# Optimization experiments

Hardware: AMD Instinct MI355X
Metric: run time of the kernel (lower is better)

The kernel has to match this reference:

```python
import jax, jax.numpy as jnp
import numpy as np

N_NODES = 50000
D = 128            # input_dim == hidden_dim == output_dim
N_EDGES = 800000   # 2 relation types concatenated
BN_EPS = 1e-5


def _gcn_conv(x, W, b, src, dst, n):
    # PyG GCNConv: add self loops, symmetric normalization, gather-scatter aggregate.
    h = x @ W                                   # [N, D]
    loop = jnp.arange(n)
    s = jnp.concatenate([src, loop])
    d = jnp.concatenate([dst, loop])
    deg = jax.ops.segment_sum(jnp.ones_like(s, dtype=h.dtype), d, num_segments=n)
    dinv = jnp.where(deg > 0, jax.lax.rsqrt(deg), 0.0)
    norm = dinv[s] * dinv[d]                    # [E+N]
    agg = jax.ops.segment_sum(h[s] * norm[:, None], d, num_segments=n)  # [N, D]
    return agg + b


def _batch_norm(x, gamma, beta):
    # BatchNorm1d training-mode math (biased variance over node axis)
    m = x.mean(axis=0)
    v = x.var(axis=0)
    return (x - m) * jax.lax.rsqrt(v + BN_EPS) * gamma + beta


def _gcn_layer(x, src, dst, W, b, gamma, beta, n):
    h = _gcn_conv(x, W, b, src, dst, n)
    h = jax.nn.relu(_batch_norm(h, gamma, beta))
    return h + x  # residual (in_features == out_features); dropout = identity (eval)


def setup_inputs() -> dict:
    key = jax.random.key(0)
    ks = jax.random.split(key, 8)
    x = jax.random.normal(ks[0], (N_NODES, D), dtype=jnp.float32)
    edge_index = jax.random.randint(ks[1], (2, N_EDGES), 0, N_NODES, dtype=jnp.int64)
    sc = 1.0 / np.sqrt(D)
    return {
        "x": x,
        "edge_index": edge_index,
        "W1": jax.random.normal(ks[2], (D, D), dtype=jnp.float32) * sc,
        "b1": jnp.zeros((D,), dtype=jnp.float32),
        "g1": jnp.ones((D,), dtype=jnp.float32),
        "be1": jnp.zeros((D,), dtype=jnp.float32),
        "W2": jax.random.normal(ks[3], (D, D), dtype=jnp.float32) * sc,
        "b2": jnp.zeros((D,), dtype=jnp.float32),
        "g2": jnp.ones((D,), dtype=jnp.float32),
        "be2": jnp.zeros((D,), dtype=jnp.float32),
        "Wa": jax.random.normal(ks[4], (D, 1), dtype=jnp.float32) * sc,
        "ba": jnp.zeros((1,), dtype=jnp.float32),
    }


def reference(x, edge_index, W1, b1, g1, be1, W2, b2, g2, be2, Wa, ba):
    n = x.shape[0]
    src, dst = edge_index[0], edge_index[1]
    h = _gcn_layer(x, src, dst, W1, b1, g1, be1, n)
    h = _gcn_layer(h, src, dst, W2, b2, g2, be2, n)
    att = jax.nn.softmax(jnp.tanh(h @ Wa + ba), axis=0)  # softmax over nodes
    return h * att
```

## Files before the change

kernel.cpp:

```cpp
#include <hip/hip_runtime.h>
#include <hip/hip_fp16.h>

#define NN 50000
#define DD 128
#define NE 800000
#define BN_EPS 1e-5f
#define NBUCK 196
#define TILE_A 4096

typedef _Float16 f16x8 __attribute__((ext_vector_type(8)));
typedef float f32x4 __attribute__((ext_vector_type(4)));

__global__ void k_hist(const int* __restrict__ dst, int* __restrict__ cnt, int ne) {
    int i = blockIdx.x * blockDim.x + threadIdx.x;
    if (i < ne) atomicAdd(&cnt[dst[i]], 1);
}

__global__ __launch_bounds__(256) void k_bsum(const int* __restrict__ cnt,
                                              int* __restrict__ bsum, int n) {
    __shared__ int red[256];
    int i = blockIdx.x * 256 + threadIdx.x;
    int v = (i < n) ? cnt[i] : 0;
    red[threadIdx.x] = v;
    __syncthreads();
    for (int off = 128; off > 0; off >>= 1) {
        if (threadIdx.x < off) red[threadIdx.x] += red[threadIdx.x + off];
        __syncthreads();
    }
    if (threadIdx.x == 0) bsum[blockIdx.x] = red[0];
}

__global__ __launch_bounds__(256) void k_bscan(int* __restrict__ bsum, int nb) {
    __shared__ int sh[256];
    int t = threadIdx.x;
    sh[t] = (t < nb) ? bsum[t] : 0;
    __syncthreads();
    for (int off = 1; off < 256; off <<= 1) {
        int add = (t >= off) ? sh[t - off] : 0;
        __syncthreads();
        sh[t] += add;
        __syncthreads();
    }
    if (t < nb) bsum[t] = sh[t];
}

__global__ __launch_bounds__(256) void k_rowp(const int* __restrict__ cnt,
                                              const int* __restrict__ bsum,
                                              int* __restrict__ rowp,
                                              int* __restrict__ cursor,
                                              int* __restrict__ bucketCur,
                                              float* __restrict__ dinv,
                                              float* __restrict__ sumsZ, int n) {
    if (blockIdx.x == 0) {
        for (int i = threadIdx.x; i < 8256; i += 256) sumsZ[i] = 0.f;
    }
    __shared__ int sh[256];
    int t = threadIdx.x;
    int i = blockIdx.x * 256 + t;
    int v = (i < n) ? cnt[i] : 0;
    sh[t] = v;
    __syncthreads();
    for (int off = 1; off < 256; off <<= 1) {
        int add = (t >= off) ? sh[t - off] : 0;
        __syncthreads();
        sh[t] += add;
        __syncthreads();
    }
    int base = (blockIdx.x > 0) ? bsum[blockIdx.x - 1] : 0;
    int excl = base + sh[t] - v;
    if (i < n) {
        rowp[i] = excl;
        cursor[i] = excl;
        dinv[i] = 1.0f / sqrtf((float)(v + 1));
        if ((i & 255) == 0) bucketCur[i >> 8] = excl;
        if (i == n - 1) rowp[n] = excl + v;
    }
}

__global__ __launch_bounds__(256) void k_binA(const int* __restrict__ src,
                                              const int* __restrict__ dst,
                                              const float* __restrict__ dinv,
                                              int* __restrict__ bucketCur,
                                              uint2* __restrict__ evS, int ne) {
    __shared__ int hcnt[NBUCK];
    __shared__ int hbase[NBUCK];
    int tid = threadIdx.x;
    for (int i = tid; i < NBUCK; i += 256) hcnt[i] = 0;
    __syncthreads();
    int base = blockIdx.x * TILE_A;
    int lim = ne - base;
    if (lim > TILE_A) lim = TILE_A;
    for (int i = tid; i < lim; i += 256) {
        int d = dst[base + i];
        atomicAdd(&hcnt[d >> 8], 1);
    }
    __syncthreads();
    for (int b = tid; b < NBUCK; b += 256) {
        hbase[b] = atomicAdd(&bucketCur[b], hcnt[b]);
        hcnt[b] = 0;
    }
    __syncthreads();
    for (int i = tid; i < lim; i += 256) {
        int d = dst[base + i];
        int s = src[base + i];
        int bk = d >> 8;
        int rank = atomicAdd(&hcnt[bk], 1);
        int pos = hbase[bk] + rank;
        unsigned short hv = __half_as_ushort(__float2half_rn(dinv[s]));
        evS[pos] = make_uint2((unsigned)s | ((unsigned)(d & 255) << 16),
                              (unsigned)hv);
    }
}

__global__ __launch_bounds__(256) void k_binB(const uint2* __restrict__ evS,
                                              const int* __restrict__ rowp,
                                              int* __restrict__ cursor,
                                              unsigned* __restrict__ ev, int n) {
    int b = blockIdx.x;
    int node0 = b << 8;
    int lo = rowp[node0];
    int nhi = node0 + 256;
    if (nhi > n) nhi = n;
    int hi = rowp[nhi];
    for (int p = lo + (int)threadIdx.x; p < hi; p += 256) {
        uint2 r = evS[p];
        int node = node0 + (int)(r.x >> 16);
        int pos = atomicAdd(&cursor[node], 1);
        ev[pos] = (r.x & 0xFFFFu) | (r.y << 16);
    }
}

__global__ __launch_bounds__(256) void k_wprep(const float* __restrict__ W1,
                                               const float* __restrict__ W2,
                                               __half* __restrict__ Wf) {
    int widx = blockIdx.x & 1;
    const float* W = widx ? W2 : W1;
    __half* outp = Wf + (size_t)widx * DD * DD;
    int s = (blockIdx.x >> 1) * 256 + threadIdx.x;
    int l = s & 63;
    int ks = (s >> 6) & 3;
    int cb = s >> 8;
    int col = cb * 16 + (l & 15);
    int kbase = ks * 32 + (l >> 4) * 8;
    __align__(16) __half tmp[8];
    #pragma unroll
    for (int j = 0; j < 8; j++) tmp[j] = __float2half_rn(W[(kbase + j) * DD + col]);
    *(uint4*)(outp + s * 8) = *(uint4*)tmp;
}

#define GTILE 64
__global__ __launch_bounds__(256) void k_gemm(const float* __restrict__ A,
                                              const __half* __restrict__ Wf,
                                              __half* __restrict__ C, int n) {
    __shared__ __half sW[DD * DD];
    __shared__ __half sA[GTILE * DD];
    int tid = threadIdx.x;
    int wave = tid >> 6;
    int lane = tid & 63;

    {
        const float4* wg = (const float4*)Wf;
        float4* ws = (float4*)sW;
        for (int i = tid; i < DD * DD / 8; i += 256) ws[i] = wg[i];
    }

    int ntiles = (n + GTILE - 1) / GTILE;
    for (int t = blockIdx.x; t < ntiles; t += gridDim.x) {
        int row0 = t * GTILE;
        __syncthreads();
        {
            const float4* Av = (const float4*)(A + (size_t)row0 * DD);
            for (int i = tid; i < GTILE * DD / 4; i += 256) {
                int r = i >> 5;
                int kq = i & 31;
                float4 v = make_float4(0.f, 0.f, 0.f, 0.f);
                if (row0 + r < n) v = Av[i];
                __half2 p0 = __floats2half2_rn(v.x, v.y);
                __half2 p1 = __floats2half2_rn(v.z, v.w);
                uint2 pk;
                pk.x = *(unsigned*)&p0;
                pk.y = *(unsigned*)&p1;
                int slot = ((r >> 4) * 4 + (kq >> 3)) * 64 +
                           (((kq >> 1) & 3) << 4) + (r & 15);
                int byte = slot * 16 + (kq & 1) * 8;
                byte ^= ((byte >> 9) & 7) << 4;
                *(uint2*)((char*)sA + byte) = pk;
            }
        }
        __syncthreads();

        f32x4 acc[8];
        #pragma unroll
        for (int cb = 0; cb < 8; cb++) acc[cb] = (f32x4)(0.0f);
        f16x8 af[4];
        #pragma unroll
        for (int ks = 0; ks < 4; ks++) {
            int rb = ((wave * 4 + ks) * 64 + lane) * 16;
            rb ^= ((rb >> 9) & 7) << 4;
            af[ks] = *(const f16x8*)((const char*)sA + rb);
        }
        #pragma unroll
        for (int cb = 0; cb < 8; cb++) {
            #pragma unroll
            for (int ks = 0; ks < 4; ks++) {
                f16x8 bf = *(const f16x8*)(sW + ((cb * 4 + ks) * 64 + lane) * 8);
                acc[cb] = __builtin_amdgcn_mfma_f32_16x16x32_f16(af[ks], bf,
                                                                 acc[cb], 0, 0, 0);
            }
        }

        __half* sC = sA + wave * (16 * DD);
        #pragma unroll
        for (int cb = 0; cb < 8; cb++) {
            int col = cb * 16 + (lane & 15);
            #pragma unroll
            for (int rr = 0; rr < 4; rr++) {
                int grow = (lane >> 4) * 4 + rr;
                sC[grow * DD + (col ^ ((grow & 3) << 4))] = __float2half(acc[cb][rr]);
            }
        }
        __syncthreads();
        #pragma unroll
        for (int i2 = 0; i2 < 4; i2++) {
            int o = (i2 * 64 + lane) * 8;
            int grow = o >> 7;
            int col0 = o & 127;
            int row = row0 + wave * 16 + grow;
            if (row < n) {
                uint4 val = *(uint4*)(sC + grow * DD + (col0 ^ ((grow & 3) << 4)));
                *(uint4*)(C + (size_t)row * DD + col0) = val;
            }
        }
    }
}

__global__ __launch_bounds__(256) void k_agg(const __half* __restrict__ h,
                                             const int* __restrict__ rowp,
                                             const unsigned* __restrict__ ev,
                                             const float* __restrict__ dinv,
                                             const float* __restrict__ bias,
                                             float* __restrict__ out,
                                             float* __restrict__ sums, int n) {
    int tid = threadIdx.x;
    int grp = tid >> 4;
    int m = tid & 15;
    int node = blockIdx.x * 16 + grp;
    bool activ = node < n;

    int beg = 0, end = 0;
    float di = 0.f;
    if (activ) { beg = rowp[node]; end = rowp[node + 1]; di = dinv[node]; }

    float sf[8] = {0.f, 0.f, 0.f, 0.f, 0.f, 0.f, 0.f, 0.f};
    float bf[8];
    {
        float4 b0 = *(const float4*)(bias + m * 8);
        float4 b1 = *(const float4*)(bias + m * 8 + 4);
        bf[0] = b0.x; bf[1] = b0.y; bf[2] = b0.z; bf[3] = b0.w;
        bf[4] = b1.x; bf[5] = b1.y; bf[6] = b1.z; bf[7] = b1.w;
        if (activ) {
            float4 raw = *(const float4*)(h + (size_t)node * DD + m * 8);
            const __half2* hp = (const __half2*)&raw;
            float2 s0 = __half22float2(hp[0]);
            float2 s1 = __half22float2(hp[1]);
            float2 s2 = __half22float2(hp[2]);
            float2 s3 = __half22float2(hp[3]);
            sf[0] = s0.x; sf[1] = s0.y; sf[2] = s1.x; sf[3] = s1.y;
            sf[4] = s2.x; sf[5] = s2.y; sf[6] = s3.x; sf[7] = s3.y;
        }
    }

    float a[8] = {0.f, 0.f, 0.f, 0.f, 0.f, 0.f, 0.f, 0.f};
    #pragma unroll 4
    for (int e = beg; e < end; e++) {
        unsigned r = ev[e];
        int s = r & 0xFFFF;
        float ww = __half2float(__ushort_as_half((unsigned short)(r >> 16)));
        float4 raw = *(const float4*)(h + (size_t)s * DD + m * 8);
        const __half2* hp = (const __half2*)&raw;
        float2 c0 = __half22float2(hp[0]);
        float2 c1 = __half22float2(hp[1]);
        float2 c2 = __half22float2(hp[2]);
        float2 c3 = __half22float2(hp[3]);
        a[0] += ww * c0.x; a[1] += ww * c0.y;
        a[2] += ww * c1.x; a[3] += ww * c1.y;
        a[4] += ww * c2.x; a[5] += ww * c2.y;
        a[6] += ww * c3.x; a[7] += ww * c3.y;
    }

    float o[8];
    float dii = di * di;
    #pragma unroll
    for (int j = 0; j < 8; j++) o[j] = di * a[j] + dii * sf[j] + bf[j];
    if (activ) {
        float* op = out + (size_t)node * DD + m * 8;
        *(float4*)op = make_float4(o[0], o[1], o[2], o[3]);
        *(float4*)(op + 4) = make_float4(o[4], o[5], o[6], o[7]);
    }

    __shared__ float rs[16][132];
    #pragma unroll
    for (int j = 0; j < 8; j++) rs[grp][m * 8 + j] = activ ? o[j] : 0.f;
    __syncthreads();

    int bank = blockIdx.x & 15;
    if (tid < 128) {
        float s = 0.f;
        #pragma unroll
        for (int r2 = 0; r2 < 16; r2++) s += rs[r2][tid];
        atomicAdd(&sums[bank * 256 + tid], s);
    } else {
        int f = tid - 128;
        float q = 0.f;
        #pragma unroll
        for (int r2 = 0; r2 < 16; r2++) { float v = rs[r2][f]; q += v * v; }
        atomicAdd(&sums[bank * 256 + 128 + f], q);
    }
}

__global__ __launch_bounds__(256) void k_bn(const float* __restrict__ X,
                                            const float* __restrict__ res,
                                            const float* __restrict__ sums,
                                            const float* __restrict__ gamma,
                                            const float* __restrict__ beta,
                                            const float* __restrict__ Wa,
                                            const float* __restrict__ ba,
                                            float* __restrict__ out,
                                            float* __restrict__ evec,
                                            float* __restrict__ Zb, int n) {
    __shared__ float s_scale[128], s_shift[128];
    if (threadIdx.x < 128) {
        int ff = threadIdx.x;
        float ssum = 0.f, qsum = 0.f;
        #pragma unroll
        for (int b = 0; b < 16; b++) {
            ssum += sums[b * 256 + ff];
            qsum += sums[b * 256 + 128 + ff];
        }
        float inv_n = 1.0f / (float)n;
        float mean = ssum * inv_n;
        float var = qsum * inv_n - mean * mean;
        float sc = gamma[ff] * (1.0f / sqrtf(var + BN_EPS));
        s_scale[ff] = sc;
        s_shift[ff] = beta[ff] - mean * sc;
    }
    __syncthreads();
    int idx = blockIdx.x * 256 + threadIdx.x;
    int total = n * (DD / 4);
    int f = (threadIdx.x & 31) * 4;
    float o[4] = {0.f, 0.f, 0.f, 0.f};
    if (idx < total) {
        float4 v = ((const float4*)X)[idx];
        float4 rv = ((const float4*)res)[idx];
        float vi[4] = {v.x, v.y, v.z, v.w};
        float ri[4] = {rv.x, rv.y, rv.z, rv.w};
        #pragma unroll
        for (int j = 0; j < 4; j++) {
            float x = vi[j] * s_scale[f + j] + s_shift[f + j];
            x = fmaxf(x, 0.f);
            o[j] = x + ri[j];
        }
        ((float4*)out)[idx] = make_float4(o[0], o[1], o[2], o[3]);
    }
    if (Wa != nullptr) {
        float t = 0.f;
        if (idx < total) {
            float4 wv = *(const float4*)(Wa + f);
            t = o[0] * wv.x + o[1] * wv.y + o[2] * wv.z + o[3] * wv.w;
        }
        #pragma unroll
        for (int m = 16; m >= 1; m >>= 1) t += __shfl_xor(t, m);
        __shared__ float part[8];
        if ((threadIdx.x & 31) == 0) {
            float ev = 0.f;
            if (idx < total) {
                ev = expf(tanhf(t + ba[0]));
                evec[idx >> 5] = ev;
            }
            part[threadIdx.x >> 5] = ev;
        }
        __syncthreads();
        if (threadIdx.x == 0) {
            float z = part[0] + part[1] + part[2] + part[3] +
                      part[4] + part[5] + part[6] + part[7];
            atomicAdd(&Zb[blockIdx.x & 63], z);
        }
    }
}

__global__ __launch_bounds__(256) void k_out(const float* __restrict__ H,
                                             const float* __restrict__ evec,
                                             const float* __restrict__ Zb,
                                             float* __restrict__ out, int n) {
    __shared__ float sZ;
    if (threadIdx.x == 0) {
        float z = 0.f;
        #pragma unroll
        for (int i = 0; i < 64; i++) z += Zb[i];
        sZ = z;
    }
    __syncthreads();
    int idx = blockIdx.x * blockDim.x + threadIdx.x;
    int total = n * (DD / 4);
    if (idx >= total) return;
    int node = idx >> 5;
    float s = evec[node] / sZ;
    float4 h = ((const float4*)H)[idx];
    ((float4*)out)[idx] = make_float4(h.x * s, h.y * s, h.z * s, h.w * s);
}

extern "C" void kernel_launch(void* const* d_in, const int* in_sizes, int n_in,
                              void* d_out, int out_size, void* d_ws, size_t ws_size,
                              hipStream_t stream) {
    const float* x   = (const float*)d_in[0];
    const int* eidx  = (const int*)d_in[1];
    const float* W1  = (const float*)d_in[2];
    const float* b1  = (const float*)d_in[3];
    const float* g1  = (const float*)d_in[4];
    const float* be1 = (const float*)d_in[5];
    const float* W2  = (const float*)d_in[6];
    const float* b2  = (const float*)d_in[7];
    const float* g2  = (const float*)d_in[8];
    const float* be2 = (const float*)d_in[9];
    const float* Wa  = (const float*)d_in[10];
    const float* ba  = (const float*)d_in[11];
    float* out = (float*)d_out;

    const int* srcp = eidx;
    const int* dstp = eidx + NE;

    float* bufA = (float*)d_ws;
    float* bufB = bufA + (size_t)NN * DD;
    float* bufC = bufB + (size_t)NN * DD;
    unsigned* ev = (unsigned*)(bufC + (size_t)NN * DD);
    float* dinv = (float*)(ev + NE);
    float* evec = dinv + NN;
    float* sums = evec + NN;
    float* Zb   = sums + 8192;
    int* cnt    = (int*)(Zb + 64);
    int* rowp   = cnt + NN;
    int* cursor = rowp + NN + 64;
    int* bsum   = cursor + NN;
    int* bucketCur = bsum + 256;
    __half* Wf  = (__half*)(bucketCur + 256);

    __half* hH  = (__half*)bufA;
    uint2* evS  = (uint2*)bufB;

    float* sumsL1 = sums;
    float* sumsL2 = sums + 4096;

    const int nscan = (NN + 255) / 256;

    k_wprep<<<16, 256, 0, stream>>>(W1, W2, Wf);

    hipMemsetAsync(cnt, 0, (size_t)NN * sizeof(int), stream);
    k_hist<<<(NE + 255) / 256, 256, 0, stream>>>(dstp, cnt, NE);
    k_bsum<<<nscan, 256, 0, stream>>>(cnt, bsum, NN);
    k_bscan<<<1, 256, 0, stream>>>(bsum, nscan);
    k_rowp<<<nscan, 256, 0, stream>>>(cnt, bsum, rowp, cursor, bucketCur, dinv,
                                      sums, NN);
    k_binA<<<(NE + TILE_A - 1) / TILE_A, 256, 0, stream>>>(srcp, dstp, dinv,
                                                           bucketCur, evS, NE);
    k_binB<<<NBUCK, 256, 0, stream>>>(evS, rowp, cursor, ev, NN);

    int gemm_grid = (NN + GTILE - 1) / GTILE;
    int agg_grid  = (NN + 15) / 16;
    int ew_grid   = (NN * (DD / 4) + 255) / 256;

    k_gemm<<<gemm_grid, 256, 0, stream>>>(x, Wf, hH, NN);
    k_agg<<<agg_grid, 256, 0, stream>>>(hH, rowp, ev, dinv, b1, bufB, sumsL1, NN);
    k_bn<<<ew_grid, 256, 0, stream>>>(bufB, x, sumsL1, g1, be1, nullptr, nullptr,
                                      bufC, nullptr, nullptr, NN);

    k_gemm<<<gemm_grid, 256, 0, stream>>>(bufC, Wf + (size_t)DD * DD, hH, NN);
    k_agg<<<agg_grid, 256, 0, stream>>>(hH, rowp, ev, dinv, b2, bufB, sumsL2, NN);
    k_bn<<<ew_grid, 256, 0, stream>>>(bufB, bufC, sumsL2, g2, be2, Wa, ba,
                                      bufC, evec, Zb, NN);

    k_out<<<ew_grid, 256, 0, stream>>>(bufC, evec, Zb, out, NN);
}
```

Measured before the change: 318.4 us.

## Fuse layer-1 BatchNorm/ReLU/residual into GEMM prologue and degree-sort aggregation nodes

```diff
diff --git a/kernel.cpp b/kernel.cpp
--- a/kernel.cpp
+++ b/kernel.cpp
@@ -50,12 +50,15 @@
                                               int* __restrict__ cursor,
                                               int* __restrict__ bucketCur,
                                               float* __restrict__ dinv,
-                                              float* __restrict__ sumsZ, int n) {
+                                              float* __restrict__ sumsZ,
+                                              int* __restrict__ dcnt, int n) {
     if (blockIdx.x == 0) {
         for (int i = threadIdx.x; i < 8256; i += 256) sumsZ[i] = 0.f;
     }
     __shared__ int sh[256];
+    __shared__ int dh[64];
     int t = threadIdx.x;
+    if (t < 64) dh[t] = 0;
     int i = blockIdx.x * 256 + t;
     int v = (i < n) ? cnt[i] : 0;
     sh[t] = v;
@@ -74,6 +77,50 @@
         dinv[i] = 1.0f / sqrtf((float)(v + 1));
         if ((i & 255) == 0) bucketCur[i >> 8] = excl;
         if (i == n - 1) rowp[n] = excl + v;
+        atomicAdd(&dh[v > 63 ? 63 : v], 1);
+    }
+    __syncthreads();
+    if (t < 64 && dh[t]) atomicAdd(&dcnt[t], dh[t]);
+}
+
+__global__ __launch_bounds__(64) void k_dscan(const int* __restrict__ dcnt,
+                                              int* __restrict__ dcur) {
+    __shared__ int sh[64];
+    int t = threadIdx.x;
+    sh[t] = dcnt[t];
+    __syncthreads();
+    for (int off = 1; off < 64; off <<= 1) {
+        int add = (t >= off) ? sh[t - off] : 0;
+        __syncthreads();
+        sh[t] += add;
+        __syncthreads();
+    }
+    dcur[t] = sh[t] - dcnt[t];
+}
+
+__global__ __launch_bounds__(256) void k_dperm(const int* __restrict__ cnt,
+                                               int* __restrict__ dcur,
+                                               int* __restrict__ perm, int n) {
+    __shared__ int dh[64], db[64];
+    int t = threadIdx.x;
+    if (t < 64) dh[t] = 0;
+    __syncthreads();
+    int i = blockIdx.x * 256 + t;
+    int b = 0;
+    if (i < n) {
+        int v = cnt[i];
+        b = v > 63 ? 63 : v;
+        atomicAdd(&dh[b], 1);
+    }
+    __syncthreads();
+    if (t < 64) {
+        db[t] = dh[t] ? atomicAdd(&dcur[t], dh[t]) : 0;
+        dh[t] = 0;
+    }
+    __syncthreads();
+    if (i < n) {
+        int r = atomicAdd(&dh[b], 1);
+        perm[db[b] + r] = i;
     }
 }
 
@@ -150,19 +197,40 @@
 
 #define GTILE 64
 __global__ __launch_bounds__(256) void k_gemm(const float* __restrict__ A,
+                                              const float* __restrict__ res,
+                                              const float* __restrict__ sums,
+                                              const float* __restrict__ gamma,
+                                              const float* __restrict__ beta,
+                                              float* __restrict__ Hout,
                                               const __half* __restrict__ Wf,
                                               __half* __restrict__ C, int n) {
     __shared__ __half sW[DD * DD];
     __shared__ __half sA[GTILE * DD];
+    __shared__ float s_scale[DD], s_shift[DD];
     int tid = threadIdx.x;
     int wave = tid >> 6;
     int lane = tid & 63;
+    bool fused = (res != nullptr);
 
     {
         const float4* wg = (const float4*)Wf;
         float4* ws = (float4*)sW;
         for (int i = tid; i < DD * DD / 8; i += 256) ws[i] = wg[i];
     }
+    if (fused && tid < DD) {
+        float ssum = 0.f, qsum = 0.f;
+        #pragma unroll
+        for (int b = 0; b < 16; b++) {
+            ssum += sums[b * 256 + tid];
+            qsum += sums[b * 256 + 128 + tid];
+        }
+        float inv_n = 1.0f / (float)n;
+        float mean = ssum * inv_n;
+        float var = qsum * inv_n - mean * mean;
+        float sc = gamma[tid] * (1.0f / sqrtf(var + BN_EPS));
+        s_scale[tid] = sc;
+        s_shift[tid] = beta[tid] - mean * sc;
+    }
 
     int ntiles = (n + GTILE - 1) / GTILE;
     for (int t = blockIdx.x; t < ntiles; t += gridDim.x) {
@@ -170,11 +238,24 @@
         __syncthreads();
         {
             const float4* Av = (const float4*)(A + (size_t)row0 * DD);
+            const float4* Rv = (const float4*)(res + (size_t)row0 * DD);
+            float4* Hv = (float4*)(Hout + (size_t)row0 * DD);
             for (int i = tid; i < GTILE * DD / 4; i += 256) {
                 int r = i >> 5;
                 int kq = i & 31;
+                bool rowok = (row0 + r < n);
                 float4 v = make_float4(0.f, 0.f, 0.f, 0.f);
-                if (row0 + r < n) v = Av[i];
+                if (rowok) v = Av[i];
+                if (fused) {
+                    float4 rv = make_float4(0.f, 0.f, 0.f, 0.f);
+                    if (rowok) rv = Rv[i];
+                    int f4 = kq * 4;
+                    v.x = fmaxf(v.x * s_scale[f4]     + s_shift[f4],     0.f) + rv.x;
+                    v.y = fmaxf(v.y * s_scale[f4 + 1] + s_shift[f4 + 1], 0.f) + rv.y;
+                    v.z = fmaxf(v.z * s_scale[f4 + 2] + s_shift[f4 + 2], 0.f) + rv.z;
+                    v.w = fmaxf(v.w * s_scale[f4 + 3] + s_shift[f4 + 3], 0.f) + rv.w;
+                    if (rowok) Hv[i] = v;
+                }
                 __half2 p0 = __floats2half2_rn(v.x, v.y);
                 __half2 p1 = __floats2half2_rn(v.z, v.w);
                 uint2 pk;
@@ -238,14 +319,16 @@
                                              const int* __restrict__ rowp,
                                              const unsigned* __restrict__ ev,
                                              const float* __restrict__ dinv,
+                                             const int* __restrict__ perm,
                                              const float* __restrict__ bias,
                                              float* __restrict__ out,
                                              float* __restrict__ sums, int n) {
     int tid = threadIdx.x;
     int grp = tid >> 4;
     int m = tid & 15;
-    int node = blockIdx.x * 16 + grp;
-    bool activ = node < n;
+    int idx = blockIdx.x * 16 + grp;
+    bool activ = idx < n;
+    int node = activ ? perm[idx] : 0;
 
     int beg = 0, end = 0;
     float di = 0.f;
@@ -438,11 +521,14 @@
     float* sums = evec + NN;
     float* Zb   = sums + 8192;
     int* cnt    = (int*)(Zb + 64);
-    int* rowp   = cnt + NN;
+    int* dcnt   = cnt + NN;
+    int* dcur   = dcnt + 64;
+    int* rowp   = dcur + 64;
     int* cursor = rowp + NN + 64;
     int* bsum   = cursor + NN;
     int* bucketCur = bsum + 256;
-    __half* Wf  = (__half*)(bucketCur + 256);
+    int* perm   = bucketCur + 256;
+    __half* Wf  = (__half*)(perm + NN);
 
     __half* hH  = (__half*)bufA;
     uint2* evS  = (uint2*)bufB;
@@ -454,27 +540,31 @@
 
     k_wprep<<<16, 256, 0, stream>>>(W1, W2, Wf);
 
-    hipMemsetAsync(cnt, 0, (size_t)NN * sizeof(int), stream);
+    hipMemsetAsync(cnt, 0, (size_t)(NN + 64) * sizeof(int), stream);
     k_hist<<<(NE + 255) / 256, 256, 0, stream>>>(dstp, cnt, NE);
     k_bsum<<<nscan, 256, 0, stream>>>(cnt, bsum, NN);
     k_bscan<<<1, 256, 0, stream>>>(bsum, nscan);
     k_rowp<<<nscan, 256, 0, stream>>>(cnt, bsum, rowp, cursor, bucketCur, dinv,
-                                      sums, NN);
+                                      sums, dcnt, NN);
     k_binA<<<(NE + TILE_A - 1) / TILE_A, 256, 0, stream>>>(srcp, dstp, dinv,
                                                            bucketCur, evS, NE);
     k_binB<<<NBUCK, 256, 0, stream>>>(evS, rowp, cursor, ev, NN);
+    k_dscan<<<1, 64, 0, stream>>>(dcnt, dcur);
+    k_dperm<<<nscan, 256, 0, stream>>>(cnt, dcur, perm, NN);
 
     int gemm_grid = (NN + GTILE - 1) / GTILE;
     int agg_grid  = (NN + 15) / 16;
     int ew_grid   = (NN * (DD / 4) + 255) / 256;
 
-    k_gemm<<<gemm_grid, 256, 0, stream>>>(x, Wf, hH, NN);
-    k_agg<<<agg_grid, 256, 0, stream>>>(hH, rowp, ev, dinv, b1, bufB, sumsL1, NN);
-    k_bn<<<ew_grid, 256, 0, stream>>>(bufB, x, sumsL1, g1, be1, nullptr, nullptr,
-                                      bufC, nullptr, nullptr, NN);
-
-    k_gemm<<<gemm_grid, 256, 0, stream>>>(bufC, Wf + (size_t)DD * DD, hH, NN);
-    k_agg<<<agg_grid, 256, 0, stream>>>(hH, rowp, ev, dinv, b2, bufB, sumsL2, NN);
+    k_gemm<<<gemm_grid, 256, 0, stream>>>(x, nullptr, nullptr, nullptr, nullptr,
+                                          nullptr, Wf, hH, NN);
+    k_agg<<<agg_grid, 256, 0, stream>>>(hH, rowp, ev, dinv, perm, b1, bufB,
+                                        sumsL1, NN);
+
+    k_gemm<<<gemm_grid, 256, 0, stream>>>(bufB, x, sumsL1, g1, be1, bufC,
+                                          Wf + (size_t)DD * DD, hH, NN);
+    k_agg<<<agg_grid, 256, 0, stream>>>(hH, rowp, ev, dinv, perm, b2, bufB,
+                                        sumsL2, NN);
     k_bn<<<ew_grid, 256, 0, stream>>>(bufB, bufC, sumsL2, g2, be2, Wa, ba,
                                       bufC, evec, Zb, NN);
 
```

New measurement: 320.1 us. Within noise of the previous version (+0.5%).

## Fuse layer-1 BatchNorm into layer-2 GEMM and prescale rows by dinv

Applied to the files above, without the earlier changes.

```diff
diff --git a/kernel.cpp b/kernel.cpp
--- a/kernel.cpp
+++ b/kernel.cpp
@@ -79,9 +79,8 @@
 
 __global__ __launch_bounds__(256) void k_binA(const int* __restrict__ src,
                                               const int* __restrict__ dst,
-                                              const float* __restrict__ dinv,
                                               int* __restrict__ bucketCur,
-                                              uint2* __restrict__ evS, int ne) {
+                                              unsigned* __restrict__ evS, int ne) {
     __shared__ int hcnt[NBUCK];
     __shared__ int hbase[NBUCK];
     int tid = threadIdx.x;
@@ -105,14 +104,11 @@
         int s = src[base + i];
         int bk = d >> 8;
         int rank = atomicAdd(&hcnt[bk], 1);
-        int pos = hbase[bk] + rank;
-        unsigned short hv = __half_as_ushort(__float2half_rn(dinv[s]));
-        evS[pos] = make_uint2((unsigned)s | ((unsigned)(d & 255) << 16),
-                              (unsigned)hv);
-    }
-}
-
-__global__ __launch_bounds__(256) void k_binB(const uint2* __restrict__ evS,
+        evS[hbase[bk] + rank] = (unsigned)s | ((unsigned)(d & 255) << 16);
+    }
+}
+
+__global__ __launch_bounds__(256) void k_binB(const unsigned* __restrict__ evS,
                                               const int* __restrict__ rowp,
                                               int* __restrict__ cursor,
                                               unsigned* __restrict__ ev, int n) {
@@ -123,10 +119,10 @@
     if (nhi > n) nhi = n;
     int hi = rowp[nhi];
     for (int p = lo + (int)threadIdx.x; p < hi; p += 256) {
-        uint2 r = evS[p];
-        int node = node0 + (int)(r.x >> 16);
+        unsigned r = evS[p];
+        int node = node0 + (int)(r >> 16);
         int pos = atomicAdd(&cursor[node], 1);
-        ev[pos] = (r.x & 0xFFFFu) | (r.y << 16);
+        ev[pos] = r & 0xFFFFu;
     }
 }
 
@@ -150,19 +146,41 @@
 
 #define GTILE 64
 __global__ __launch_bounds__(256) void k_gemm(const float* __restrict__ A,
+                                              const float* __restrict__ res,
+                                              const float* __restrict__ sums,
+                                              const float* __restrict__ gamma,
+                                              const float* __restrict__ beta,
+                                              float* __restrict__ Hout,
+                                              const float* __restrict__ dscale,
                                               const __half* __restrict__ Wf,
                                               __half* __restrict__ C, int n) {
     __shared__ __half sW[DD * DD];
     __shared__ __half sA[GTILE * DD];
+    __shared__ float s_scale[DD], s_shift[DD];
     int tid = threadIdx.x;
     int wave = tid >> 6;
     int lane = tid & 63;
+    bool fused = (res != nullptr);
 
     {
         const float4* wg = (const float4*)Wf;
         float4* ws = (float4*)sW;
         for (int i = tid; i < DD * DD / 8; i += 256) ws[i] = wg[i];
     }
+    if (fused && tid < DD) {
+        float ssum = 0.f, qsum = 0.f;
+        #pragma unroll
+        for (int b = 0; b < 16; b++) {
+            ssum += sums[b * 256 + tid];
+            qsum += sums[b * 256 + 128 + tid];
+        }
+        float inv_n = 1.0f / (float)n;
+        float mean = ssum * inv_n;
+        float var = qsum * inv_n - mean * mean;
+        float sc = gamma[tid] * (1.0f / sqrtf(var + BN_EPS));
+        s_scale[tid] = sc;
+        s_shift[tid] = beta[tid] - mean * sc;
+    }
 
     int ntiles = (n + GTILE - 1) / GTILE;
     for (int t = blockIdx.x; t < ntiles; t += gridDim.x) {
@@ -170,11 +188,24 @@
         __syncthreads();
         {
             const float4* Av = (const float4*)(A + (size_t)row0 * DD);
+            const float4* Rv = (const float4*)(res + (size_t)row0 * DD);
+            float4* Hv = (float4*)(Hout + (size_t)row0 * DD);
             for (int i = tid; i < GTILE * DD / 4; i += 256) {
                 int r = i >> 5;
                 int kq = i & 31;
+                bool rowok = (row0 + r < n);
                 float4 v = make_float4(0.f, 0.f, 0.f, 0.f);
-                if (row0 + r < n) v = Av[i];
+                if (rowok) v = Av[i];
+                if (fused) {
+                    float4 rv = make_float4(0.f, 0.f, 0.f, 0.f);
+                    if (rowok) rv = Rv[i];
+                    int f4 = kq * 4;
+                    v.x = fmaxf(v.x * s_scale[f4]     + s_shift[f4],     0.f) + rv.x;
+                    v.y = fmaxf(v.y * s_scale[f4 + 1] + s_shift[f4 + 1], 0.f) + rv.y;
+                    v.z = fmaxf(v.z * s_scale[f4 + 2] + s_shift[f4 + 2], 0.f) + rv.z;
+                    v.w = fmaxf(v.w * s_scale[f4 + 3] + s_shift[f4 + 3], 0.f) + rv.w;
+                    if (rowok) Hv[i] = v;
+                }
                 __half2 p0 = __floats2half2_rn(v.x, v.y);
                 __half2 p1 = __floats2half2_rn(v.z, v.w);
                 uint2 pk;
@@ -209,6 +240,13 @@
             }
         }
 
+        float dv[4];
+        #pragma unroll
+        for (int rr = 0; rr < 4; rr++) {
+            int row = row0 + wave * 16 + (lane >> 4) * 4 + rr;
+            dv[rr] = (row < n) ? dscale[row] : 1.f;
+        }
+
         __half* sC = sA + wave * (16 * DD);
         #pragma unroll
         for (int cb = 0; cb < 8; cb++) {
@@ -216,7 +254,8 @@
             #pragma unroll
             for (int rr = 0; rr < 4; rr++) {
                 int grow = (lane >> 4) * 4 + rr;
-                sC[grow * DD + (col ^ ((grow & 3) << 4))] = __float2half(acc[cb][rr]);
+                sC[grow * DD + (col ^ ((grow & 3) << 4))] =
+                    __float2half(acc[cb][rr] * dv[rr]);
             }
         }
         __syncthreads();
@@ -233,6 +272,12 @@
         }
     }
 }
+
+#define ACC8(raw) { const __half2* hp_ = (const __half2*)&(raw);               \
+    float2 c0_ = __half22float2(hp_[0]); float2 c1_ = __half22float2(hp_[1]);  \
+    float2 c2_ = __half22float2(hp_[2]); float2 c3_ = __half22float2(hp_[3]);  \
+    a[0] += c0_.x; a[1] += c0_.y; a[2] += c1_.x; a[3] += c1_.y;                \
+    a[4] += c2_.x; a[5] += c2_.y; a[6] += c3_.x; a[7] += c3_.y; }
 
 __global__ __launch_bounds__(256) void k_agg(const __half* __restrict__ h,
                                              const int* __restrict__ rowp,
@@ -271,27 +316,36 @@
     }
 
     float a[8] = {0.f, 0.f, 0.f, 0.f, 0.f, 0.f, 0.f, 0.f};
-    #pragma unroll 4
-    for (int e = beg; e < end; e++) {
-        unsigned r = ev[e];
-        int s = r & 0xFFFF;
-        float ww = __half2float(__ushort_as_half((unsigned short)(r >> 16)));
+    int e = beg;
+    int cnt4 = (end - beg) >> 2;
+    if (cnt4 > 0) {
+        unsigned s0 = ev[e], s1 = ev[e + 1], s2 = ev[e + 2], s3 = ev[e + 3];
+        float4 r0 = *(const float4*)(h + (size_t)s0 * DD + m * 8);
+        float4 r1 = *(const float4*)(h + (size_t)s1 * DD + m * 8);
+        float4 r2 = *(const float4*)(h + (size_t)s2 * DD + m * 8);
+        float4 r3 = *(const float4*)(h + (size_t)s3 * DD + m * 8);
+        for (int g = 1; g < cnt4; g++) {
+            e += 4;
+            unsigned t0 = ev[e], t1 = ev[e + 1], t2 = ev[e + 2], t3 = ev[e + 3];
+            float4 q0 = *(const float4*)(h + (size_t)t0 * DD + m * 8);
+            float4 q1 = *(const float4*)(h + (size_t)t1 * DD + m * 8);
+            float4 q2 = *(const float4*)(h + (size_t)t2 * DD + m * 8);
+            float4 q3 = *(const float4*)(h + (size_t)t3 * DD + m * 8);
+            ACC8(r0); ACC8(r1); ACC8(r2); ACC8(r3);
+            r0 = q0; r1 = q1; r2 = q2; r3 = q3;
+        }
+        ACC8(r0); ACC8(r1); ACC8(r2); ACC8(r3);
+        e += 4;
+    }
+    for (; e < end; e++) {
+        unsigned s = ev[e];
         float4 raw = *(const float4*)(h + (size_t)s * DD + m * 8);
-        const __half2* hp = (const __half2*)&raw;
-        float2 c0 = __half22float2(hp[0]);
-        float2 c1 = __half22float2(hp[1]);
-        float2 c2 = __half22float2(hp[2]);
-        float2 c3 = __half22float2(hp[3]);
-        a[0] += ww * c0.x; a[1] += ww * c0.y;
-        a[2] += ww * c1.x; a[3] += ww * c1.y;
-        a[4] += ww * c2.x; a[5] += ww * c2.y;
-        a[6] += ww * c3.x; a[7] += ww * c3.y;
+        ACC8(raw);
     }
 
     float o[8];
-    float dii = di * di;
     #pragma unroll
-    for (int j = 0; j < 8; j++) o[j] = di * a[j] + dii * sf[j] + bf[j];
+    for (int j = 0; j < 8; j++) o[j] = di * (a[j] + sf[j]) + bf[j];
     if (activ) {
         float* op = out + (size_t)node * DD + m * 8;
         *(float4*)op = make_float4(o[0], o[1], o[2], o[3]);
@@ -445,7 +499,7 @@
     __half* Wf  = (__half*)(bucketCur + 256);
 
     __half* hH  = (__half*)bufA;
-    uint2* evS  = (uint2*)bufB;
+    unsigned* evS = (unsigned*)bufB;
 
     float* sumsL1 = sums;
     float* sumsL2 = sums + 4096;
@@ -460,7 +514,7 @@
     k_bscan<<<1, 256, 0, stream>>>(bsum, nscan);
     k_rowp<<<nscan, 256, 0, stream>>>(cnt, bsum, rowp, cursor, bucketCur, dinv,
                                       sums, NN);
-    k_binA<<<(NE + TILE_A - 1) / TILE_A, 256, 0, stream>>>(srcp, dstp, dinv,
+    k_binA<<<(NE + TILE_A - 1) / TILE_A, 256, 0, stream>>>(srcp, dstp,
                                                            bucketCur, evS, NE);
     k_binB<<<NBUCK, 256, 0, stream>>>(evS, rowp, cursor, ev, NN);
 
@@ -468,12 +522,12 @@
     int agg_grid  = (NN + 15) / 16;
     int ew_grid   = (NN * (DD / 4) + 255) / 256;
 
-    k_gemm<<<gemm_grid, 256, 0, stream>>>(x, Wf, hH, NN);
+    k_gemm<<<gemm_grid, 256, 0, stream>>>(x, nullptr, nullptr, nullptr, nullptr,
+                                          nullptr, dinv, Wf, hH, NN);
     k_agg<<<agg_grid, 256, 0, stream>>>(hH, rowp, ev, dinv, b1, bufB, sumsL1, NN);
-    k_bn<<<ew_grid, 256, 0, stream>>>(bufB, x, sumsL1, g1, be1, nullptr, nullptr,
-                                      bufC, nullptr, nullptr, NN);
-
-    k_gemm<<<gemm_grid, 256, 0, stream>>>(bufC, Wf + (size_t)DD * DD, hH, NN);
+
+    k_gemm<<<gemm_grid, 256, 0, stream>>>(bufB, x, sumsL1, g1, be1, bufC,
+                                          dinv, Wf + (size_t)DD * DD, hH, NN);
     k_agg<<<agg_grid, 256, 0, stream>>>(hH, rowp, ev, dinv, b2, bufB, sumsL2, NN);
     k_bn<<<ew_grid, 256, 0, stream>>>(bufB, bufC, sumsL2, g2, be2, Wa, ba,
                                       bufC, evec, Zb, NN);
```

Result: no change. 315.9 us (-0.8%).
